# Kernel tuning notes

Hardware: AMD Instinct MI355X
Metric: run time of the kernel (lower is better)

The kernel has to match this reference:

```python
import jax, jax.numpy as jnp
import numpy as np

B, N, IN_DIM, HID, OUT_DIM = 8, 1024, 768, 128, 768
H1, H2, MHA_HEADS, C = 8, 1, 4, 32
ALPHA = 0.2
NEG = -9e15
LN_EPS = 1e-5


def _gat_layer(x, W, a1, a2, adj_mask):
    # x: [B,N,Fin], W: [H,Fin,Fout], a1/a2: [H,Fout], adj_mask: [B,N,N] bool
    h = jnp.einsum('bni,hio->bhno', x, W)                      # [B,H,N,F]
    s1 = jnp.einsum('bhno,ho->bhn', h, a1)                     # score for source node i
    s2 = jnp.einsum('bhno,ho->bhn', h, a2)                     # score for target node j
    e = jax.nn.leaky_relu(s1[:, :, :, None] + s2[:, :, None, :], negative_slope=ALPHA)
    e = jnp.where(adj_mask[:, None, :, :], e, NEG)
    attn = jax.nn.softmax(e, axis=-1)                          # [B,H,N,N]
    hp = jnp.einsum('bhnm,bhmo->bhno', attn, h)                # [B,H,N,F]
    b, nh, n, f = hp.shape
    return hp.transpose(0, 2, 1, 3).reshape(b, n, nh * f)      # concat heads -> [B,N,H*F]


def _mha(q, k, v, wq, bq, wk, bk, wv, bv, wo, bo, n_heads):
    # torch-style MultiheadAttention (eval, no dropout). q:[B,Lq,E] k,v:[B,Lk,E]
    b, lq, e = q.shape
    lk = k.shape[1]
    hd = e // n_heads
    Q = (q @ wq + bq).reshape(b, lq, n_heads, hd).transpose(0, 2, 1, 3)
    K = (k @ wk + bk).reshape(b, lk, n_heads, hd).transpose(0, 2, 1, 3)
    V = (v @ wv + bv).reshape(b, lk, n_heads, hd).transpose(0, 2, 1, 3)
    scores = jnp.einsum('bhqd,bhkd->bhqk', Q, K) / jnp.sqrt(jnp.float32(hd))
    attn = jax.nn.softmax(scores, axis=-1)
    out = jnp.einsum('bhqk,bhkd->bhqd', attn, V)
    out = out.transpose(0, 2, 1, 3).reshape(b, lq, e)
    return out @ wo + bo


def _layernorm(x, g, b):
    mu = jnp.mean(x, axis=-1, keepdims=True)
    var = jnp.var(x, axis=-1, keepdims=True)
    return (x - mu) * jax.lax.rsqrt(var + LN_EPS) * g + b


def setup_inputs() -> dict:
    key = jax.random.key(0)
    ks = jax.random.split(key, 24)
    s = lambda fan_in: 1.0 / np.sqrt(fan_in)
    inp = {
        'node_features': jax.random.normal(ks[0], (B, N, IN_DIM), jnp.float32),
        'adjacency': jax.random.randint(ks[1], (B, N, N), 0, 2, jnp.int32),
        'context_indices': jax.random.randint(ks[2], (B, C), 0, N, jnp.int32),
        # GAT layer 1: 8 heads, in=768 -> out=128 each
        'W1': jax.random.normal(ks[3], (H1, IN_DIM, HID), jnp.float32) * s(IN_DIM),
        'a1_1': jax.random.normal(ks[4], (H1, HID), jnp.float32) * s(2 * HID),
        'a2_1': jax.random.normal(ks[5], (H1, HID), jnp.float32) * s(2 * HID),
        # GAT layer 2: 1 head, in=1024 -> out=128
        'W2': jax.random.normal(ks[6], (H2, HID * H1, HID), jnp.float32) * s(HID * H1),
        'a1_2': jax.random.normal(ks[7], (H2, HID), jnp.float32) * s(2 * HID),
        'a2_2': jax.random.normal(ks[8], (H2, HID), jnp.float32) * s(2 * HID),
        # query MultiheadAttention (embed_dim=128, 4 heads)
        'wq': jax.random.normal(ks[9], (HID, HID), jnp.float32) * s(HID),
        'bq': jnp.zeros((HID,), jnp.float32),
        'wk': jax.random.normal(ks[10], (HID, HID), jnp.float32) * s(HID),
        'bk': jnp.zeros((HID,), jnp.float32),
        'wv': jax.random.normal(ks[11], (HID, HID), jnp.float32) * s(HID),
        'bv': jnp.zeros((HID,), jnp.float32),
        'wo': jax.random.normal(ks[12], (HID, HID), jnp.float32) * s(HID),
        'bo': jnp.zeros((HID,), jnp.float32),
        # projection MLP
        'p1_w': jax.random.normal(ks[13], (HID, HID), jnp.float32) * s(HID),
        'p1_b': jnp.zeros((HID,), jnp.float32),
        'ln_g': jnp.ones((HID,), jnp.float32),
        'ln_b': jnp.zeros((HID,), jnp.float32),
        'p2_w': jax.random.normal(ks[14], (HID, OUT_DIM), jnp.float32) * s(HID),
        'p2_b': jnp.zeros((OUT_DIM,), jnp.float32),
    }
    return inp


def reference(node_features, adjacency, context_indices,
              W1, a1_1, a2_1, W2, a1_2, a2_2,
              wq, bq, wk, bk, wv, bv, wo, bo,
              p1_w, p1_b, ln_g, ln_b, p2_w, p2_b):
    adj_mask = adjacency > 0
    h = jax.nn.elu(_gat_layer(node_features, W1, a1_1, a2_1, adj_mask))  # [B,N,1024]
    h = jax.nn.elu(_gat_layer(h, W2, a1_2, a2_2, adj_mask))              # [B,N,128]
    q = h[:, 0:1, :]                                                      # [B,1,E]
    ctx = jnp.take_along_axis(h, context_indices[:, :, None], axis=1)     # [B,C,E]
    pooled = _mha(q, ctx, ctx, wq, bq, wk, bk, wv, bv, wo, bo, MHA_HEADS)[:, 0, :]
    z = jax.nn.relu(_layernorm(pooled @ p1_w + p1_b, ln_g, ln_b))
    return z @ p2_w + p2_b                                                # [B,OUT_DIM]
```

## Files before the change

### kernel.cpp

```cpp
#include <hip/hip_runtime.h>
#include <hip/hip_bf16.h>

#define ALPHA 0.2f
#define LOG2E 1.4426950408889634f

using short8  = __attribute__((ext_vector_type(8))) short;
using short4v = __attribute__((ext_vector_type(4))) short;
using f32x4   = __attribute__((ext_vector_type(4))) float;
using int4v   = __attribute__((ext_vector_type(4))) int;

static __device__ __forceinline__ float b2f(short s) {
    union { float f; unsigned u; } v; v.u = ((unsigned)(unsigned short)s) << 16; return v.f;
}
static __device__ __forceinline__ short f2bf(float f) {
    __hip_bfloat16 h = __float2bfloat16(f);
    return *reinterpret_cast<short*>(&h);
}
static __device__ __forceinline__ float fexp2(float x) {
    return __builtin_amdgcn_exp2f(x);
}
static __device__ __forceinline__ void gload_lds16(const void* g, void* l) {
    __builtin_amdgcn_global_load_lds(
        (const __attribute__((address_space(1))) unsigned*)g,
        (__attribute__((address_space(3))) unsigned*)l, 16, 0, 0);
}

__global__ __launch_bounds__(256) void k_prep(
        const int* __restrict__ adj, unsigned* __restrict__ adjb,
        const float* __restrict__ x, short* __restrict__ xb,
        const float* __restrict__ W1, short* __restrict__ W1T,
        const float* __restrict__ W2, short* __restrict__ W2T) {
    int bid = blockIdx.x, t = threadIdx.x;
    if (bid < 32768) {
        int idx = bid * 256 + t;
        int lane = t & 63;
        unsigned long long m = __ballot(adj[idx] > 0);
        if ((lane & 31) == 0) adjb[idx >> 5] = (unsigned)(m >> (lane & 32));
    } else if (bid < 38912) {
        int idx = (bid - 32768) * 256 + t;
        f32x4 v = ((const f32x4*)x)[idx];
        short4v o;
        o[0] = f2bf(v[0]); o[1] = f2bf(v[1]); o[2] = f2bf(v[2]); o[3] = f2bf(v[3]);
        ((short4v*)xb)[idx] = o;
    } else if (bid < 41984) {
        int idx = (bid - 38912) * 256 + t;
        int n = idx / 768, k = idx - n * 768;
        int h = n >> 7, o = n & 127;
        W1T[idx] = f2bf(W1[(h * 768 + k) * 128 + o]);
    } else {
        int idx = (bid - 41984) * 256 + t;
        int n = idx >> 10, k = idx & 1023;
        W2T[idx] = f2bf(W2[k * 128 + n]);
    }
}

__global__ __launch_bounds__(256) void k_gemm_bt(
        const short* __restrict__ A, const short* __restrict__ Bt,
        short* __restrict__ Ct, int K, int Ncols,
        const float* __restrict__ a1, const float* __restrict__ a2,
        float* __restrict__ s1, float* __restrict__ s2) {
    int tid = threadIdx.x, wave = tid >> 6, lane = tid & 63;
    int lr = lane & 15, lg = lane >> 4;
    int flat = blockIdx.y * gridDim.x + blockIdx.x;
    int chunkw = (gridDim.x * gridDim.y) >> 3;
    int swz = (flat & 7) * chunkw + (flat >> 3);
    int bx = swz % gridDim.x, by = swz / gridDim.x;
    int m0 = bx * 128, n0 = by * 128;
    int wm = (wave >> 1) * 64, wn = (wave & 1) * 64;
    __shared__ short lsA[2][128 * 64], lsB[2][128 * 64];
    __shared__ float sred1[2][128], sred2[2][128];
    f32x4 acc[4][4];
#pragma unroll
    for (int i = 0; i < 4; i++)
#pragma unroll
        for (int j = 0; j < 4; j++) acc[i][j] = (f32x4){0.f, 0.f, 0.f, 0.f};

    auto stage = [&](int bufsel, int k0) {
#pragma unroll
        for (int s = 0; s < 4; s++) {
            int chunk = s * 256 + tid;
            int r = chunk >> 3, c = chunk & 7;
            int csrc = c ^ (r & 7);
            gload_lds16(A + (size_t)(m0 + r) * K + k0 + csrc * 8, &lsA[bufsel][chunk * 8]);
            gload_lds16(Bt + (size_t)(n0 + r) * K + k0 + csrc * 8, &lsB[bufsel][chunk * 8]);
        }
    };
    auto compute = [&](const short* la, const short* lb) {
#pragma unroll
        for (int kk = 0; kk < 2; kk++) {
            short8 a[4], bb[4];
#pragma unroll
            for (int f = 0; f < 4; f++) {
                int ra = wm + f * 16 + lr, rb = wn + f * 16 + lr;
                a[f]  = *(const short8*)(la + ra * 64 + (((kk * 4 + lg) ^ (ra & 7)) * 8));
                bb[f] = *(const short8*)(lb + rb * 64 + (((kk * 4 + lg) ^ (rb & 7)) * 8));
            }
#pragma unroll
            for (int fm = 0; fm < 4; fm++)
#pragma unroll
                for (int fn = 0; fn < 4; fn++)
                    acc[fm][fn] = __builtin_amdgcn_mfma_f32_16x16x32_bf16(a[fm], bb[fn], acc[fm][fn], 0, 0, 0);
        }
    };
    stage(0, 0);
    __syncthreads();
    for (int k2 = 0; k2 < K; k2 += 128) {
        stage(1, k2 + 64);
        compute(lsA[0], lsB[0]);
        __syncthreads();
        if (k2 + 128 < K) stage(0, k2 + 128);
        compute(lsA[1], lsB[1]);
        __syncthreads();
    }
    short* stg = &lsA[0][0];
#pragma unroll
    for (int fm = 0; fm < 4; fm++) {
#pragma unroll
        for (int fn = 0; fn < 4; fn++) {
            int nl = wn + fn * 16 + lr;
            int i4w = (wm + fm * 16 + lg * 4) >> 2;
            short4v st;
            st[0] = f2bf(acc[fm][fn][0]); st[1] = f2bf(acc[fm][fn][1]);
            st[2] = f2bf(acc[fm][fn][2]); st[3] = f2bf(acc[fm][fn][3]);
            *(short4v*)(stg + (nl * 32 + (i4w ^ (nl & 31))) * 4) = st;
        }
    }
    __syncthreads();
    size_t gbase = ((size_t)(m0 >> 10) * Ncols + n0) * 1024 + (m0 & 1023);
#pragma unroll
    for (int it = 0; it < 8; it++) {
        int idx8 = it * 256 + tid;
        int nl = idx8 >> 4, p = idx8 & 15;
        int i4a = 2 * p, i4b = 2 * p + 1;
        short4v lo = *(short4v*)(stg + (nl * 32 + (i4a ^ (nl & 31))) * 4);
        short4v hi = *(short4v*)(stg + (nl * 32 + (i4b ^ (nl & 31))) * 4);
        short8 v;
#pragma unroll
        for (int r = 0; r < 4; r++) { v[r] = lo[r]; v[r + 4] = hi[r]; }
        *(short8*)(Ct + gbase + (size_t)nl * 1024 + p * 8) = v;
    }
    if (a1 != nullptr) {
        int h = by;
        float av1[4], av2[4];
#pragma unroll
        for (int fn = 0; fn < 4; fn++) {
            int o = wn + fn * 16 + lr;
            av1[fn] = a1[h * 128 + o];
            av2[fn] = a2[h * 128 + o];
        }
        int wcol = wave & 1;
#pragma unroll
        for (int fm = 0; fm < 4; fm++)
#pragma unroll
            for (int r = 0; r < 4; r++) {
                float v1 = acc[fm][0][r] * av1[0] + acc[fm][1][r] * av1[1]
                         + acc[fm][2][r] * av1[2] + acc[fm][3][r] * av1[3];
                float v2 = acc[fm][0][r] * av2[0] + acc[fm][1][r] * av2[1]
                         + acc[fm][2][r] * av2[2] + acc[fm][3][r] * av2[3];
#pragma unroll
                for (int off = 1; off < 16; off <<= 1) {
                    v1 += __shfl_xor(v1, off);
                    v2 += __shfl_xor(v2, off);
                }
                if (lr == 0) {
                    int il = wm + fm * 16 + lg * 4 + r;
                    sred1[wcol][il] = v1;
                    sred2[wcol][il] = v2;
                }
            }
        __syncthreads();
        if (tid < 128) {
            int b = m0 >> 10;
            int irow = (b * 8 + h) * 1024 + (m0 & 1023) + tid;
            s1[irow] = (sred1[0][tid] + sred1[1][tid]) * LOG2E;
            s2[irow] = (sred2[0][tid] + sred2[1][tid]) * LOG2E;
        }
    }
}

__global__ __launch_bounds__(256) void k_gemm64(
        const short* __restrict__ A, const short* __restrict__ Bt,
        short* __restrict__ Ct, int K, int Ncols) {
    int tid = threadIdx.x, wave = tid >> 6, lane = tid & 63;
    int lr = lane & 15, lg = lane >> 4;
    int flat = blockIdx.y * gridDim.x + blockIdx.x;
    int chunkw = (gridDim.x * gridDim.y) >> 3;
    int swz = (flat & 7) * chunkw + (flat >> 3);
    int bx = swz % gridDim.x, by = swz / gridDim.x;
    int m0 = bx * 64, n0 = by * 64;
    int wm = (wave >> 1) * 32, wn = (wave & 1) * 32;
    __shared__ short lsA[2][64 * 32], lsB[2][64 * 32];
    f32x4 acc[2][2];
#pragma unroll
    for (int i = 0; i < 2; i++)
#pragma unroll
        for (int j = 0; j < 2; j++) acc[i][j] = (f32x4){0.f, 0.f, 0.f, 0.f};

    auto stage = [&](int bufsel, int k0) {
        int r = tid >> 2, c = tid & 3;
        int csrc = c ^ (r & 3);
        int base = (wave * 64) * 8;
        gload_lds16(A + (size_t)(m0 + r) * K + k0 + csrc * 8, &lsA[bufsel][base]);
        gload_lds16(Bt + (size_t)(n0 + r) * K + k0 + csrc * 8, &lsB[bufsel][base]);
    };
    stage(0, 0);
    __syncthreads();
    int buf = 0;
    for (int k0 = 0; k0 < K; k0 += 32) {
        if (k0 + 32 < K) stage(buf ^ 1, k0 + 32);
        short8 a[2], bb[2];
#pragma unroll
        for (int f = 0; f < 2; f++) {
            int ra = wm + f * 16 + lr, rb = wn + f * 16 + lr;
            a[f]  = *(const short8*)(&lsA[buf][ra * 32 + ((lg ^ (ra & 3)) * 8)]);
            bb[f] = *(const short8*)(&lsB[buf][rb * 32 + ((lg ^ (rb & 3)) * 8)]);
        }
#pragma unroll
        for (int fm = 0; fm < 2; fm++)
#pragma unroll
            for (int fn = 0; fn < 2; fn++)
                acc[fm][fn] = __builtin_amdgcn_mfma_f32_16x16x32_bf16(a[fm], bb[fn], acc[fm][fn], 0, 0, 0);
        __syncthreads();
        buf ^= 1;
    }
#pragma unroll
    for (int fm = 0; fm < 2; fm++) {
        int mb = m0 + wm + fm * 16 + lg * 4;
        size_t obase = ((size_t)(mb >> 10) * Ncols) * 1024 + (mb & 1023);
#pragma unroll
        for (int fn = 0; fn < 2; fn++) {
            int n = n0 + wn + fn * 16 + lr;
            short4v st;
            st[0] = f2bf(acc[fm][fn][0]); st[1] = f2bf(acc[fm][fn][1]);
            st[2] = f2bf(acc[fm][fn][2]); st[3] = f2bf(acc[fm][fn][3]);
            *(short4v*)(Ct + obase + (size_t)n * 1024) = st;
        }
    }
}

__global__ __launch_bounds__(512) void k_attn1(
        const short* __restrict__ ht, const unsigned* __restrict__ adjb,
        const float* __restrict__ s1, const float* __restrict__ s2,
        short* __restrict__ out) {
    int flat = blockIdx.y * 8 + blockIdx.x;
    int swz = (flat & 7) * 64 + (flat >> 3);
    int bh = swz >> 3, bxi = swz & 7;
    int b = bh >> 3, h = bh & 7;
    int tid = threadIdx.x, wave = tid >> 6, lane = tid & 63;
    int lr = lane & 15, lg = lane >> 4;
    int ic = bxi * 128 + wave * 16 + lr;
    int row = bh * 1024 + ic;
    float s1i = s1[row];
    const unsigned long long* abrow =
        (const unsigned long long*)(adjb + ((size_t)(b << 10) + ic) * 32);
    const float* s2r = s2 + bh * 1024;
    const short* hbase = ht + (size_t)bh * 131072;

    __shared__ short lsh[2][16384];
    __shared__ float ls2[1024];
    f32x4 acc[8];
#pragma unroll
    for (int f = 0; f < 8; f++) acc[f] = (f32x4){0.f, 0.f, 0.f, 0.f};
    f32x4 accs = (f32x4){0.f, 0.f, 0.f, 0.f};
    short8 ones8;
#pragma unroll
    for (int e = 0; e < 8; e++) ones8[e] = (short)0x3F80;

    auto stage = [&](int bufsel, int j0) {
#pragma unroll
        for (int s = 0; s < 4; s++) {
            int chunk = s * 512 + tid;
            int r = chunk >> 4, c = chunk & 15;
            int csrc = c ^ (r & 15);
            gload_lds16(hbase + (size_t)r * 1024 + j0 + csrc * 8,
                        &lsh[bufsel][chunk * 8]);
        }
    };
    auto compute = [&](const short* ls, int j0) {
        unsigned long long aw0 = abrow[j0 >> 6], aw1 = abrow[(j0 >> 6) + 1];
#pragma unroll
        for (int kk = 0; kk < 4; kk++) {
            int jb = j0 + kk * 32 + lg * 8;
            f32x4 t0 = *(const f32x4*)(&ls2[jb]);
            f32x4 t1 = *(const f32x4*)(&ls2[jb + 4]);
            unsigned long long aw = (kk < 2) ? aw0 : aw1;
            unsigned bits = (unsigned)(aw >> ((kk & 1) * 32 + lg * 8)) & 0xFFu;
            float pv[8];
#pragma unroll
            for (int e = 0; e < 8; e++) {
                float sv = e < 4 ? t0[e] : t1[e & 3];
                float ee = s1i + sv;
                ee = fmaxf(ee, ALPHA * ee);
                float p = fexp2(ee);
                pv[e] = ((bits >> e) & 1) ? p : 0.f;
            }
            int4v pw;
#pragma unroll
            for (int w = 0; w < 4; w++) {
                int d;
                asm("v_cvt_pk_bf16_f32 %0, %1, %2"
                    : "=v"(d) : "v"(pv[2 * w]), "v"(pv[2 * w + 1]));
                pw[w] = d;
            }
            short8 pb = __builtin_bit_cast(short8, pw);
            accs = __builtin_amdgcn_mfma_f32_16x16x32_bf16(ones8, pb, accs, 0, 0, 0);
#pragma unroll
            for (int fm = 0; fm < 8; fm++) {
                int r = fm * 16 + lr;
                int ck = (kk * 4 + lg) ^ (r & 15);
                short8 af = *(const short8*)(ls + r * 128 + ck * 8);
                acc[fm] = __builtin_amdgcn_mfma_f32_16x16x32_bf16(af, pb, acc[fm], 0, 0, 0);
            }
        }
    };

    if (wave < 4) {
        gload_lds16(s2r + (size_t)(wave * 64 + lane) * 4, &ls2[wave * 256]);
    }
    stage(0, 0);
    __syncthreads();
    for (int t2 = 0; t2 < 1024; t2 += 256) {
        stage(1, t2 + 128);
        compute(lsh[0], t2);
        __syncthreads();
        if (t2 + 256 < 1024) stage(0, t2 + 256);
        compute(lsh[1], t2 + 128);
        __syncthreads();
    }
    float rdi = 1.f / accs[0];
    size_t orow = ((size_t)(b << 10) + ic) * 1024 + h * 128;
#pragma unroll
    for (int fm = 0; fm < 8; fm++) {
        int ob = (fm << 4) + lg * 4;
        short4v st;
#pragma unroll
        for (int r = 0; r < 4; r++) {
            float x = acc[fm][r] * rdi;
            x = x > 0.f ? x : expm1f(x);
            st[r] = f2bf(x);
        }
        *(short4v*)(out + orow + ob) = st;
    }
}

__global__ __launch_bounds__(256) void k_attn2g(
        const short* __restrict__ h2t, const unsigned* __restrict__ adjb,
        const float* __restrict__ a1, const float* __restrict__ a2,
        const int* __restrict__ cidx, float* __restrict__ ghat) {
    int tile = blockIdx.x;
    int b = blockIdx.y;
    int tid = threadIdx.x, wave = tid >> 6, lane = tid & 63;
    int lr = lane & 15, lg = lane >> 4;

    __shared__ int nodes[16];
    __shared__ float ss1[16];
    __shared__ float sp1[16][17];
    __shared__ float ls2q[1024];
    __shared__ float sps[4][16];
    __shared__ float sacc[4][16][129];

    const short* hb = h2t + (size_t)b * 131072;

    if (tid < 16) {
        int pos = tile * 16 + tid;
        int nd0 = 0;
        if (pos >= 1 && pos <= 32) nd0 = cidx[b * 32 + pos - 1];
        nodes[tid] = nd0;
    }
    {
        int j4 = wave * 256 + lane * 4;
        const short* base = hb + j4;
        f32x4 a2v = {0.f, 0.f, 0.f, 0.f};
#pragma unroll 8
        for (int o = 0; o < 128; o++) {
            short4v v = *(const short4v*)(base + ((size_t)o << 10));
            float w2 = a2[o];
#pragma unroll
            for (int r = 0; r < 4; r++) a2v[r] += b2f(v[r]) * w2;
        }
#pragma unroll
        for (int r = 0; r < 4; r++) a2v[r] *= LOG2E;
        *(f32x4*)(&ls2q[j4]) = a2v;
    }
    __syncthreads();
    {
        int nd1 = nodes[tid & 15];
        int oc = tid >> 4;
        float p1 = 0.f;
#pragma unroll
        for (int oo = 0; oo < 8; oo++) {
            int o = oc * 8 + oo;
            p1 += b2f(hb[((size_t)o << 10) + nd1]) * a1[o];
        }
        sp1[oc][tid & 15] = p1;
    }
    __syncthreads();
    if (tid < 16) {
        float s = 0.f;
#pragma unroll
        for (int oc = 0; oc < 16; oc++) s += sp1[oc][tid];
        ss1[tid] = s * LOG2E;
    }
    __syncthreads();

    int nd = nodes[lr];
    float s1i = ss1[lr];
    const unsigned long long* abrow =
        (const unsigned long long*)(adjb + ((size_t)(b << 10) + nd) * 32);
    f32x4 acc[8];
#pragma unroll
    for (int f = 0; f < 8; f++) acc[f] = (f32x4){0.f, 0.f, 0.f, 0.f};
    float psum = 0.f;

    for (int j0 = wave * 256; j0 < wave * 256 + 256; j0 += 32) {
        int jb = j0 + lg * 8;
        f32x4 t0 = *(const f32x4*)(&ls2q[jb]);
        f32x4 t1 = *(const f32x4*)(&ls2q[jb + 4]);
        unsigned bits = (unsigned)(abrow[j0 >> 6] >> ((j0 & 32) + lg * 8)) & 0xFFu;
        short8 pb;
#pragma unroll
        for (int e = 0; e < 8; e++) {
            float sv = e < 4 ? t0[e] : t1[e & 3];
            float ee = s1i + sv;
            ee = fmaxf(ee, ALPHA * ee);
            float p = fexp2(ee);
            p = ((bits >> e) & 1) ? p : 0.f;
            psum += p;
            pb[e] = f2bf(p);
        }
#pragma unroll
        for (int fm = 0; fm < 8; fm++) {
            short8 af = *(const short8*)(hb + (size_t)(fm * 16 + lr) * 1024 + jb);
            acc[fm] = __builtin_amdgcn_mfma_f32_16x16x32_bf16(af, pb, acc[fm], 0, 0, 0);
        }
    }
    psum += __shfl_xor(psum, 16);
    psum += __shfl_xor(psum, 32);
    if (lg == 0) sps[wave][lr] = psum;
#pragma unroll
    for (int fm = 0; fm < 8; fm++)
#pragma unroll
        for (int r = 0; r < 4; r++)
            sacc[wave][lr][fm * 16 + lg * 4 + r] = acc[fm][r];
    __syncthreads();
    for (int e = tid; e < 2048; e += 256) {
        int li = e >> 7, o = e & 127;
        float sum = sps[0][li] + sps[1][li] + sps[2][li] + sps[3][li];
        float v = (sacc[0][li][o] + sacc[1][li][o] + sacc[2][li][o] + sacc[3][li][o]) / sum;
        v = v > 0.f ? v : expm1f(v);
        ghat[((size_t)b * 48 + tile * 16 + li) * 128 + o] = v;
    }
}

__global__ __launch_bounds__(256) void k_qkv(
        const float* __restrict__ ghat,
        const float* __restrict__ wk, const float* __restrict__ bk,
        const float* __restrict__ wvp, const float* __restrict__ bv,
        float* __restrict__ Kp, float* __restrict__ Vp) {
    int b = blockIdx.y, rg = blockIdx.x & 7, o0 = (blockIdx.x >> 3) * 64;
    int t = threadIdx.x, wvi = t >> 6, ln = t & 63;
    __shared__ float sx[4][128];
    __shared__ float sWk[128 * 64], sWv[128 * 64];

    if (wvi < 2) {
        int cb = wvi * 64;
        gload_lds16(ghat + ((size_t)b * 48 + 1 + rg * 4) * 128 + (size_t)(cb + ln) * 4,
                    (float*)sx + cb * 4);
    }
#pragma unroll
    for (int s = 0; s < 8; s++) {
        int cb = s * 256 + wvi * 64;
        int q = cb + ln, rw = q >> 4, c4 = q & 15;
        gload_lds16(wk  + (size_t)rw * 128 + o0 + c4 * 4, &sWk[cb * 4]);
        gload_lds16(wvp + (size_t)rw * 128 + o0 + c4 * 4, &sWv[cb * 4]);
    }
    __syncthreads();
    int o = o0 + ln;
    float ka = bk[o], va = bv[o];
#pragma unroll 32
    for (int c = 0; c < 128; c++) {
        float x = sx[wvi][c];
        ka += x * sWk[c * 64 + ln];
        va += x * sWv[c * 64 + ln];
    }
    int r = rg * 4 + wvi;
    Kp[((size_t)b * 32 + r) * 128 + o] = ka;
    Vp[((size_t)b * 32 + r) * 128 + o] = va;
}

__global__ __launch_bounds__(256) void k_tail(
        const float* __restrict__ ghat, const float* __restrict__ Kp,
        const float* __restrict__ Vp,
        const float* __restrict__ wq, const float* __restrict__ bq,
        const float* __restrict__ wo, const float* __restrict__ bo,
        const float* __restrict__ p1w, const float* __restrict__ p1b,
        const float* __restrict__ lng, const float* __restrict__ lnb,
        float* __restrict__ tvec) {
    int b = blockIdx.x, t = threadIdx.x;
    int wvi = t >> 6, ln = t & 63;
    __shared__ float sq[128], sQ[128], sK[32][128], sV[32][128];
    __shared__ float sP[4][33], sO[128], sT[128], sZ[128];
    __shared__ float sred[2];
    __shared__ float sW[128 * 128];

#pragma unroll
    for (int s = 0; s < 4; s++) {
        int cb = s * 256 + wvi * 64;
        gload_lds16(Kp + (size_t)b * 4096 + (size_t)(cb + ln) * 4, (float*)sK + cb * 4);
        gload_lds16(Vp + (size_t)b * 4096 + (size_t)(cb + ln) * 4, (float*)sV + cb * 4);
    }
#pragma unroll
    for (int s = 0; s < 16; s++) {
        int cb = s * 256 + wvi * 64;
        gload_lds16(wq + (size_t)(cb + ln) * 4, &sW[cb * 4]);
    }
    if (t < 128) sq[t] = ghat[(size_t)b * 48 * 128 + t];
    __syncthreads();
    if (t < 128) {
        float a0 = 0.f, a1 = 0.f, a2 = 0.f, a3 = 0.f;
#pragma unroll
        for (int c = 0; c < 128; c += 4) {
            a0 += sq[c]     * sW[c * 128 + t];
            a1 += sq[c + 1] * sW[(c + 1) * 128 + t];
            a2 += sq[c + 2] * sW[(c + 2) * 128 + t];
            a3 += sq[c + 3] * sW[(c + 3) * 128 + t];
        }
        sQ[t] = bq[t] + ((a0 + a1) + (a2 + a3));
    }
    __syncthreads();
#pragma unroll
    for (int s = 0; s < 16; s++) {
        int cb = s * 256 + wvi * 64;
        gload_lds16(wo + (size_t)(cb + ln) * 4, &sW[cb * 4]);
    }
    if (t < 128) {
        int hh = t >> 5, jj = t & 31;
        float s = 0.f;
#pragma unroll
        for (int d = 0; d < 32; d++) s += sQ[hh * 32 + d] * sK[jj][hh * 32 + d];
        s *= 0.17677669529663687f;
        float m = s;
#pragma unroll
        for (int off = 16; off > 0; off >>= 1) m = fmaxf(m, __shfl_xor(m, off, 32));
        float p = __expf(s - m);
        float sum = p;
#pragma unroll
        for (int off = 16; off > 0; off >>= 1) sum += __shfl_xor(sum, off, 32);
        sP[hh][jj] = p / sum;
    }
    __syncthreads();
    if (t < 128) {
        int hh = t >> 5;
        float s = 0.f;
#pragma unroll
        for (int jj = 0; jj < 32; jj++) s += sP[hh][jj] * sV[jj][t];
        sO[t] = s;
    }
    __syncthreads();
    if (t < 128) {
        float a0 = 0.f, a1 = 0.f, a2 = 0.f, a3 = 0.f;
#pragma unroll
        for (int c = 0; c < 128; c += 4) {
            a0 += sO[c]     * sW[c * 128 + t];
            a1 += sO[c + 1] * sW[(c + 1) * 128 + t];
            a2 += sO[c + 2] * sW[(c + 2) * 128 + t];
            a3 += sO[c + 3] * sW[(c + 3) * 128 + t];
        }
        sT[t] = bo[t] + ((a0 + a1) + (a2 + a3));
    }
    __syncthreads();
#pragma unroll
    for (int s = 0; s < 16; s++) {
        int cb = s * 256 + wvi * 64;
        gload_lds16(p1w + (size_t)(cb + ln) * 4, &sW[cb * 4]);
    }
    __syncthreads();
    if (t < 128) {
        float a0 = 0.f, a1 = 0.f, a2 = 0.f, a3 = 0.f;
#pragma unroll
        for (int c = 0; c < 128; c += 4) {
            a0 += sT[c]     * sW[c * 128 + t];
            a1 += sT[c + 1] * sW[(c + 1) * 128 + t];
            a2 += sT[c + 2] * sW[(c + 2) * 128 + t];
            a3 += sT[c + 3] * sW[(c + 3) * 128 + t];
        }
        sZ[t] = p1b[t] + ((a0 + a1) + (a2 + a3));
    }
    __syncthreads();
    if (t < 64) {
        float v = sZ[t] + sZ[t + 64];
#pragma unroll
        for (int off = 32; off > 0; off >>= 1) v += __shfl_xor(v, off);
        if (t == 0) sred[0] = v * (1.f / 128.f);
    }
    __syncthreads();
    float mu = sred[0];
    if (t < 64) {
        float d1 = sZ[t] - mu, d2 = sZ[t + 64] - mu;
        float v = d1 * d1 + d2 * d2;
#pragma unroll
        for (int off = 32; off > 0; off >>= 1) v += __shfl_xor(v, off);
        if (t == 0) sred[1] = v * (1.f / 128.f);
    }
    __syncthreads();
    float rstd = rsqrtf(sred[1] + 1e-5f);
    if (t < 128) {
        float z = (sZ[t] - mu) * rstd * lng[t] + lnb[t];
        tvec[b * 128 + t] = fmaxf(z, 0.f);
    }
}

__global__ __launch_bounds__(256) void k_p2(
        const float* __restrict__ tvec, const float* __restrict__ p2w,
        const float* __restrict__ p2b, float* __restrict__ out) {
    int jj0 = blockIdx.x * 128, b = blockIdx.y;
    int t = threadIdx.x, wvi = t >> 6, ln = t & 63;
    __shared__ float sT[128];
    __shared__ float sW[128 * 128];

#pragma unroll
    for (int s = 0; s < 16; s++) {
        int cb = s * 256 + wvi * 64;
        int q = cb + ln, c = q >> 5, c4 = q & 31;
        gload_lds16(p2w + (size_t)c * 768 + jj0 + c4 * 4, &sW[cb * 4]);
    }
    if (t < 128) sT[t] = tvec[b * 128 + t];
    __syncthreads();
    if (t < 128) {
        float a0 = 0.f, a1 = 0.f, a2 = 0.f, a3 = 0.f;
#pragma unroll
        for (int c = 0; c < 128; c += 4) {
            a0 += sT[c]     * sW[c * 128 + t];
            a1 += sT[c + 1] * sW[(c + 1) * 128 + t];
            a2 += sT[c + 2] * sW[(c + 2) * 128 + t];
            a3 += sT[c + 3] * sW[(c + 3) * 128 + t];
        }
        out[b * 768 + jj0 + t] = p2b[jj0 + t] + ((a0 + a1) + (a2 + a3));
    }
}

extern "C" void kernel_launch(void* const* d_in, const int* in_sizes, int n_in,
                              void* d_out, int out_size, void* d_ws, size_t ws_size,
                              hipStream_t stream) {
    const float* x   = (const float*)d_in[0];
    const int*  adj  = (const int*)d_in[1];
    const int*  cidx = (const int*)d_in[2];
    const float* W1  = (const float*)d_in[3];
    const float* a11 = (const float*)d_in[4];
    const float* a21 = (const float*)d_in[5];
    const float* W2  = (const float*)d_in[6];
    const float* a12 = (const float*)d_in[7];
    const float* a22 = (const float*)d_in[8];
    const float* wq = (const float*)d_in[9];  const float* bq = (const float*)d_in[10];
    const float* wk = (const float*)d_in[11]; const float* bk = (const float*)d_in[12];
    const float* wv = (const float*)d_in[13]; const float* bv = (const float*)d_in[14];
    const float* wo = (const float*)d_in[15]; const float* bo = (const float*)d_in[16];
    const float* p1w = (const float*)d_in[17]; const float* p1b = (const float*)d_in[18];
    const float* lng = (const float*)d_in[19]; const float* lnb = (const float*)d_in[20];
    const float* p2w = (const float*)d_in[21]; const float* p2b = (const float*)d_in[22];
    float* out = (float*)d_out;

    char* ws = (char*)d_ws;
    size_t off = 0;
    auto alloc = [&](size_t bytes) -> char* {
        char* p = ws + off;
        off = (off + bytes + 255) & ~(size_t)255;
        return p;
    };
    short* Xb   = (short*)alloc(8192ull * 768 * 2);
    short* W1T  = (short*)alloc(1024ull * 768 * 2);
    short* W2T  = (short*)alloc(128ull * 1024 * 2);
    unsigned* adjb = (unsigned*)alloc(8ull * 1024 * 32 * 4);
    short* h1t  = (short*)alloc(64ull * 128 * 1024 * 2);
    float* s1a  = (float*)alloc(64ull * 1024 * 4);
    float* s2a  = (float*)alloc(64ull * 1024 * 4);
    short* hcat = (short*)alloc(8192ull * 1024 * 2);
    short* h2t  = (short*)alloc(8ull * 128 * 1024 * 2);
    float* ghat = (float*)alloc(8ull * 48 * 128 * 4);
    float* Kp   = (float*)alloc(8ull * 32 * 128 * 4);
    float* Vp   = (float*)alloc(8ull * 32 * 128 * 4);
    float* tvec = (float*)alloc(8ull * 128 * 4);
    if (off > ws_size) return;

    k_prep<<<42496, 256, 0, stream>>>(adj, adjb, x, Xb, W1, W1T, W2, W2T);

    k_gemm_bt<<<dim3(64, 8), 256, 0, stream>>>(Xb, W1T, h1t, 768, 1024,
                                               a11, a21, s1a, s2a);
    k_attn1<<<dim3(8, 64), 512, 0, stream>>>(h1t, adjb, s1a, s2a, hcat);

    k_gemm64<<<dim3(128, 2), 256, 0, stream>>>(hcat, W2T, h2t, 1024, 128);
    k_attn2g<<<dim3(3, 8), 256, 0, stream>>>(h2t, adjb, a12, a22, cidx, ghat);

    k_qkv<<<dim3(16, 8), 256, 0, stream>>>(ghat, wk, bk, wv, bv, Kp, Vp);
    k_tail<<<8, 256, 0, stream>>>(ghat, Kp, Vp, wq, bq, wo, bo,
                                  p1w, p1b, lng, lnb, tvec);
    k_p2<<<dim3(6, 8), 256, 0, stream>>>(tvec, p2w, p2b, out);
}
```

Before: 136.5 us.

## Load h fragments directly from global memory in attn1, removing LDS staging

Removes the double-buffered LDS staging of the per-head transposed feature tile in the first GAT attention kernel. Each lane instead loads its MFMA A operand directly from global memory inside the column loop, and the block-wide barriers are dropped. The aim is to cut LDS traffic and sync overhead and to raise occupancy by freeing 64 KB of LDS. The cost is that repeated global/L2 reads across the 8 waves and global load latency are no longer hidden by prefetch.

```diff
diff --git a/kernel.cpp b/kernel.cpp
--- a/kernel.cpp
+++ b/kernel.cpp
@@ -255,8 +255,8 @@
         (const unsigned long long*)(adjb + ((size_t)(b << 10) + ic) * 32);
     const float* s2r = s2 + bh * 1024;
     const short* hbase = ht + (size_t)bh * 131072;
-
-    __shared__ short lsh[2][16384];
+    const short* hlane = hbase + (size_t)lr * 1024 + lg * 8;
+
     __shared__ float ls2[1024];
     f32x4 acc[8];
 #pragma unroll
@@ -266,66 +266,40 @@
 #pragma unroll
     for (int e = 0; e < 8; e++) ones8[e] = (short)0x3F80;
 
-    auto stage = [&](int bufsel, int j0) {
-#pragma unroll
-        for (int s = 0; s < 4; s++) {
-            int chunk = s * 512 + tid;
-            int r = chunk >> 4, c = chunk & 15;
-            int csrc = c ^ (r & 15);
-            gload_lds16(hbase + (size_t)r * 1024 + j0 + csrc * 8,
-                        &lsh[bufsel][chunk * 8]);
-        }
-    };
-    auto compute = [&](const short* ls, int j0) {
-        unsigned long long aw0 = abrow[j0 >> 6], aw1 = abrow[(j0 >> 6) + 1];
-#pragma unroll
-        for (int kk = 0; kk < 4; kk++) {
-            int jb = j0 + kk * 32 + lg * 8;
-            f32x4 t0 = *(const f32x4*)(&ls2[jb]);
-            f32x4 t1 = *(const f32x4*)(&ls2[jb + 4]);
-            unsigned long long aw = (kk < 2) ? aw0 : aw1;
-            unsigned bits = (unsigned)(aw >> ((kk & 1) * 32 + lg * 8)) & 0xFFu;
-            float pv[8];
-#pragma unroll
-            for (int e = 0; e < 8; e++) {
-                float sv = e < 4 ? t0[e] : t1[e & 3];
-                float ee = s1i + sv;
-                ee = fmaxf(ee, ALPHA * ee);
-                float p = fexp2(ee);
-                pv[e] = ((bits >> e) & 1) ? p : 0.f;
-            }
-            int4v pw;
-#pragma unroll
-            for (int w = 0; w < 4; w++) {
-                int d;
-                asm("v_cvt_pk_bf16_f32 %0, %1, %2"
-                    : "=v"(d) : "v"(pv[2 * w]), "v"(pv[2 * w + 1]));
-                pw[w] = d;
-            }
-            short8 pb = __builtin_bit_cast(short8, pw);
-            accs = __builtin_amdgcn_mfma_f32_16x16x32_bf16(ones8, pb, accs, 0, 0, 0);
-#pragma unroll
-            for (int fm = 0; fm < 8; fm++) {
-                int r = fm * 16 + lr;
-                int ck = (kk * 4 + lg) ^ (r & 15);
-                short8 af = *(const short8*)(ls + r * 128 + ck * 8);
-                acc[fm] = __builtin_amdgcn_mfma_f32_16x16x32_bf16(af, pb, acc[fm], 0, 0, 0);
-            }
-        }
-    };
-
     if (wave < 4) {
         gload_lds16(s2r + (size_t)(wave * 64 + lane) * 4, &ls2[wave * 256]);
     }
-    stage(0, 0);
-    __syncthreads();
-    for (int t2 = 0; t2 < 1024; t2 += 256) {
-        stage(1, t2 + 128);
-        compute(lsh[0], t2);
-        __syncthreads();
-        if (t2 + 256 < 1024) stage(0, t2 + 256);
-        compute(lsh[1], t2 + 128);
-        __syncthreads();
+    __syncthreads();
+
+    for (int j0 = 0; j0 < 1024; j0 += 32) {
+        int jb = j0 + lg * 8;
+        f32x4 t0 = *(const f32x4*)(&ls2[jb]);
+        f32x4 t1 = *(const f32x4*)(&ls2[jb + 4]);
+        unsigned bits = (unsigned)(abrow[j0 >> 6] >> ((j0 & 32) + lg * 8)) & 0xFFu;
+        float pv[8];
+#pragma unroll
+        for (int e = 0; e < 8; e++) {
+            float sv = e < 4 ? t0[e] : t1[e & 3];
+            float ee = s1i + sv;
+            ee = fmaxf(ee, ALPHA * ee);
+            float p = fexp2(ee);
+            pv[e] = ((bits >> e) & 1) ? p : 0.f;
+        }
+        int4v pw;
+#pragma unroll
+        for (int w = 0; w < 4; w++) {
+            int d;
+            asm("v_cvt_pk_bf16_f32 %0, %1, %2"
+                : "=v"(d) : "v"(pv[2 * w]), "v"(pv[2 * w + 1]));
+            pw[w] = d;
+        }
+        short8 pb = __builtin_bit_cast(short8, pw);
+        accs = __builtin_amdgcn_mfma_f32_16x16x32_bf16(ones8, pb, accs, 0, 0, 0);
+#pragma unroll
+        for (int fm = 0; fm < 8; fm++) {
+            short8 af = *(const short8*)(hlane + (size_t)(fm << 4) * 1024 + j0);
+            acc[fm] = __builtin_amdgcn_mfma_f32_16x16x32_bf16(af, pb, acc[fm], 0, 0, 0);
+        }
     }
     float rdi = 1.f / accs[0];
     size_t orow = ((size_t)(b << 10) + ic) * 1024 + h * 128;
```

Result: slower. 236.8 us (+73.5%).

## Transpose weights via LDS tiles and deepen k_gemm64 K-step to 64

Applied to the files above, without the earlier changes.

The weight transpose-and-convert in k_prep now goes through a padded 64x64 LDS tile, so both the fp32 reads and the bf16 writes are coalesced instead of strided gathers. This also shrinks the block count for that phase. k_gemm64 now stages 64-wide K slices with an 8-way XOR swizzle, runs two MFMA k-steps per barrier, and unrolls the double buffer by two, which halves the number of barriers per K. The cost is more LDS per block (possible occupancy loss), and the loop assumes K is a multiple of 128.

```diff
diff --git a/kernel.cpp b/kernel.cpp
--- a/kernel.cpp
+++ b/kernel.cpp
@@ -42,15 +42,35 @@
         short4v o;
         o[0] = f2bf(v[0]); o[1] = f2bf(v[1]); o[2] = f2bf(v[2]); o[3] = f2bf(v[3]);
         ((short4v*)xb)[idx] = o;
-    } else if (bid < 41984) {
-        int idx = (bid - 38912) * 256 + t;
-        int n = idx / 768, k = idx - n * 768;
-        int h = n >> 7, o = n & 127;
-        W1T[idx] = f2bf(W1[(h * 768 + k) * 128 + o]);
     } else {
-        int idx = (bid - 41984) * 256 + t;
-        int n = idx >> 10, k = idx & 1023;
-        W2T[idx] = f2bf(W2[k * 128 + n]);
+        __shared__ short tileT[64][65];
+        int tb = bid - 38912;
+        const float* S; short* D; int ldS, ldD, r0, c0;
+        if (tb < 192) {
+            int hh = tb / 24, tt = tb % 24;
+            int kt = tt >> 1, ot = tt & 1;
+            S = W1 + (size_t)hh * 768 * 128; ldS = 128;
+            D = W1T + (size_t)hh * 128 * 768; ldD = 768;
+            r0 = kt * 64; c0 = ot * 64;
+        } else {
+            int tt = tb - 192;
+            int kt = tt >> 1, nt = tt & 1;
+            S = W2; ldS = 128;
+            D = W2T; ldD = 1024;
+            r0 = kt * 64; c0 = nt * 64;
+        }
+        int tr = t >> 6, tc = t & 63;
+#pragma unroll
+        for (int s = 0; s < 16; s++) {
+            int r = s * 4 + tr;
+            tileT[tc][r] = f2bf(S[(size_t)(r0 + r) * ldS + c0 + tc]);
+        }
+        __syncthreads();
+#pragma unroll
+        for (int s = 0; s < 16; s++) {
+            int dr = s * 4 + tr;
+            D[(size_t)(c0 + dr) * ldD + r0 + tc] = tileT[dr][tc];
+        }
     }
 }
 
@@ -189,7 +209,7 @@
     int bx = swz % gridDim.x, by = swz / gridDim.x;
     int m0 = bx * 64, n0 = by * 64;
     int wm = (wave >> 1) * 32, wn = (wave & 1) * 32;
-    __shared__ short lsA[2][64 * 32], lsB[2][64 * 32];
+    __shared__ short lsA[2][64 * 64], lsB[2][64 * 64];
     f32x4 acc[2][2];
 #pragma unroll
     for (int i = 0; i < 2; i++)
@@ -197,31 +217,41 @@
         for (int j = 0; j < 2; j++) acc[i][j] = (f32x4){0.f, 0.f, 0.f, 0.f};
 
     auto stage = [&](int bufsel, int k0) {
-        int r = tid >> 2, c = tid & 3;
-        int csrc = c ^ (r & 3);
-        int base = (wave * 64) * 8;
-        gload_lds16(A + (size_t)(m0 + r) * K + k0 + csrc * 8, &lsA[bufsel][base]);
-        gload_lds16(Bt + (size_t)(n0 + r) * K + k0 + csrc * 8, &lsB[bufsel][base]);
+#pragma unroll
+        for (int s = 0; s < 2; s++) {
+            int chunk = s * 256 + tid;
+            int r = chunk >> 3, c = chunk & 7;
+            int csrc = c ^ (r & 7);
+            gload_lds16(A + (size_t)(m0 + r) * K + k0 + csrc * 8, &lsA[bufsel][chunk * 8]);
+            gload_lds16(Bt + (size_t)(n0 + r) * K + k0 + csrc * 8, &lsB[bufsel][chunk * 8]);
+        }
+    };
+    auto compute = [&](const short* la, const short* lb) {
+#pragma unroll
+        for (int kk = 0; kk < 2; kk++) {
+            short8 a[2], bb[2];
+#pragma unroll
+            for (int f = 0; f < 2; f++) {
+                int ra = wm + f * 16 + lr, rb = wn + f * 16 + lr;
+                a[f]  = *(const short8*)(la + ra * 64 + (((kk * 4 + lg) ^ (ra & 7)) * 8));
+                bb[f] = *(const short8*)(lb + rb * 64 + (((kk * 4 + lg) ^ (rb & 7)) * 8));
+            }
+#pragma unroll
+            for (int fm = 0; fm < 2; fm++)
+#pragma unroll
+                for (int fn = 0; fn < 2; fn++)
+                    acc[fm][fn] = __builtin_amdgcn_mfma_f32_16x16x32_bf16(a[fm], bb[fn], acc[fm][fn], 0, 0, 0);
+        }
     };
     stage(0, 0);
     __syncthreads();
-    int buf = 0;
-    for (int k0 = 0; k0 < K; k0 += 32) {
-        if (k0 + 32 < K) stage(buf ^ 1, k0 + 32);
-        short8 a[2], bb[2];
-#pragma unroll
-        for (int f = 0; f < 2; f++) {
-            int ra = wm + f * 16 + lr, rb = wn + f * 16 + lr;
-            a[f]  = *(const short8*)(&lsA[buf][ra * 32 + ((lg ^ (ra & 3)) * 8)]);
-            bb[f] = *(const short8*)(&lsB[buf][rb * 32 + ((lg ^ (rb & 3)) * 8)]);
-        }
-#pragma unroll
-        for (int fm = 0; fm < 2; fm++)
-#pragma unroll
-            for (int fn = 0; fn < 2; fn++)
-                acc[fm][fn] = __builtin_amdgcn_mfma_f32_16x16x32_bf16(a[fm], bb[fn], acc[fm][fn], 0, 0, 0);
+    for (int k2 = 0; k2 < K; k2 += 128) {
+        stage(1, k2 + 64);
+        compute(lsA[0], lsB[0]);
         __syncthreads();
-        buf ^= 1;
+        if (k2 + 128 < K) stage(0, k2 + 128);
+        compute(lsA[1], lsB[1]);
+        __syncthreads();
     }
 #pragma unroll
     for (int fm = 0; fm < 2; fm++) {
@@ -682,7 +712,7 @@
     float* tvec = (float*)alloc(8ull * 128 * 4);
     if (off > ws_size) return;
 
-    k_prep<<<42496, 256, 0, stream>>>(adj, adjb, x, Xb, W1, W1T, W2, W2T);
+    k_prep<<<39136, 256, 0, stream>>>(adj, adjb, x, Xb, W1, W1T, W2, W2T);
 
     k_gemm_bt<<<dim3(64, 8), 256, 0, stream>>>(Xb, W1T, h1t, 768, 1024,
                                                a11, a21, s1a, s2a);
```

New measurement: 132.6 us. 2.8% less time.
